# Optimization experiments

Measured on AMD Instinct MI355X. Metric: run time of the kernel, lower is better.

## Reference

```python
import jax, jax.numpy as jnp
import numpy as np

N_CLASS = 85
BLANK = N_CLASS - 1  # blank_index = n_class - 1
ALPHA = 0.05
B, T, D = 4096, 96, 64


def setup_inputs() -> dict:
    key = jax.random.key(0)
    k1, k2, k3, k4 = jax.random.split(key, 4)
    preds = jax.random.normal(k1, (B, T, N_CLASS), dtype=jnp.float32)
    features = jax.random.normal(k2, (B, T, D), dtype=jnp.float32)
    labels = jax.random.randint(k3, (B, T), 0, N_CLASS, dtype=jnp.int32)
    centers = jax.random.normal(k4, (N_CLASS, D), dtype=jnp.float32) * 0.01
    return {"preds": preds, "features": features, "labels": labels, "centers": centers}


def _char_mask(pred_labels):
    # CTC collapse: keep non-blank positions that are the last of a repeat run.
    is_char = pred_labels != BLANK
    rep = pred_labels[:, :-1] == pred_labels[:, 1:]          # [B, T-1]
    tail = pred_labels[:, :1] > BLANK                         # always False (as in source)
    char_rep = jnp.concatenate([rep, tail], axis=1)           # [B, T]
    return is_char & jnp.logical_not(char_rep)


def reference(preds, features, labels, centers):
    # preds:    [B, T, n_class] softmax/logits -> argmax decode
    # features: [B, T, feat_dims]
    # labels:   [B, T] int, char label aligned to each timestep
    pred_labels = jnp.argmax(preds, axis=-1)                  # [B, T]
    mask = _char_mask(pred_labels).astype(features.dtype)     # [B, T] ragged-as-mask

    centers_batch = centers[labels]                           # gather -> [B, T, D]
    diff = centers_batch - features                           # [B, T, D]

    # tf.nn.l2_loss = sum(x^2)/2, restricted to valid char positions
    loss = 0.5 * jnp.sum(mask * jnp.sum(diff * diff, axis=-1))

    # unique_with_counts analog: per-class counts of valid char positions
    labels_flat = labels.reshape(-1)
    mask_flat = mask.reshape(-1)
    counts = jax.ops.segment_sum(mask_flat, labels_flat, num_segments=N_CLASS)  # [n_class]
    appear = counts[labels]                                   # [B, T]

    # alpha * diff / (1 + appear_times), zeroed outside char positions
    delta = ALPHA * diff * (mask / (1.0 + appear))[..., None]  # [B, T, D]

    # scatter_nd: centers.assign_sub(scatter of per-char deltas)
    upd = jax.ops.segment_sum(delta.reshape(-1, D), labels_flat, num_segments=N_CLASS)
    new_centers = centers - upd                               # [n_class, D]
    return loss, new_centers
```

## Files before the change

### kernel.cpp

```cpp
#include <hip/hip_runtime.h>
#include <cstdint>

#define BB     4096
#define TT     96
#define NC     85
#define BLANKC 84
#define DD     64
#define ALPHA  0.05f
#define BT     (BB * TT)
#define SLICE_F (NC * 17)
#define NF4    (TT * NC / 4)

template<int C0, int C1>
__device__ inline void scanR(const float* __restrict__ row, float& bv, int& bc) {
    bv = row[C0]; bc = C0;
#pragma unroll
    for (int c = C0 + 1; c < C1; ++c) {
        float v = row[c];
        if (v > bv) { bv = v; bc = c; }
    }
}

__global__ __launch_bounds__(512) void k_amask(const float4* __restrict__ p4,
                                               const int* __restrict__ labels,
                                               unsigned* __restrict__ labm,
                                               int* __restrict__ hpartT,
                                               float* __restrict__ out) {
    __shared__ float rows[TT * NC];
    __shared__ float sv[4 * TT];
    __shared__ int   sc[4 * TT];
    __shared__ int   pls[TT];
    __shared__ int   h[NC];
    int tid = threadIdx.x;
    int b   = blockIdx.x;
    if (tid < NC) h[tid] = 0;
    if (b == 0 && tid == 480) out[0] = 0.f;

    const float4* src = p4 + (size_t)b * NF4;
    float4* r4 = (float4*)rows;
    float4 v[4];
#pragma unroll
    for (int k = 0; k < 4; ++k)
        v[k] = src[min(tid + k * 512, NF4 - 1)];
#pragma unroll
    for (int k = 0; k < 4; ++k) {
        int i = tid + k * 512;
        if (i < NF4) r4[i] = v[k];
    }
    __syncthreads();

    int q = tid >> 7, r = tid & 127;
    if (r < TT) {
        const float* row = rows + r * NC;
        float bv; int bc;
        switch (q) {
            case 0:  scanR< 0, 22>(row, bv, bc); break;
            case 1:  scanR<22, 43>(row, bv, bc); break;
            case 2:  scanR<43, 64>(row, bv, bc); break;
            default: scanR<64, 85>(row, bv, bc); break;
        }
        sv[q * TT + r] = bv; sc[q * TT + r] = bc;
    }
    __syncthreads();
    if (tid < TT) {
        float bv = sv[tid]; int bc = sc[tid];
#pragma unroll
        for (int qq = 1; qq < 4; ++qq) {
            float v2 = sv[qq * TT + tid];
            int   c2 = sc[qq * TT + tid];
            if (v2 > bv) { bv = v2; bc = c2; }
        }
        pls[tid] = bc;
    }
    __syncthreads();
    if (tid < TT) {
        int p = pls[tid];
        int m = (p != BLANKC) && (tid == TT - 1 || p != pls[tid + 1]);
        int lab = labels[b * TT + tid];
        labm[b * TT + tid] = (unsigned)lab | ((unsigned)m << 31);
        atomicAdd(&h[lab], m);
    }
    __syncthreads();
    if (tid < NC) hpartT[tid * BB + b] = h[tid];
}

__global__ __launch_bounds__(512, 6) void k_main(const float* __restrict__ feat,
                                                 const unsigned* __restrict__ labm,
                                                 float* __restrict__ updp,
                                                 float* __restrict__ lossp, int nb) {
    __shared__ float sl[8 * SLICE_F];
    __shared__ float lred[8];
    int tid = threadIdx.x;
    for (int i = tid; i < 8 * SLICE_F; i += 512) sl[i] = 0.f;
    __syncthreads();

    int lane = tid & 63;
    int w    = tid >> 6;
    int dq   = w & 3;
    int wg   = w >> 2;
    int sub  = lane >> 4;
    int l16  = lane & 15;
    float* slice = sl + w * SLICE_F;

    int ppc = BT / (nb * 2);
    int p0  = (blockIdx.x * 2 + wg) * ppc;
    int nss = ppc / 16;
    const float* fbase = feat + dq * 16 + l16;

    float lsum = 0.f;
    float fA0, fA1, fA2, fA3, fB0, fB1, fB2, fB3;
    uint4 lA0, lA1, lA2, lA3, lB0, lB1, lB2, lB3;

#define ISSUE(P, f0, f1, f2, f3, q0, q1, q2, q3) do {            \
    int _p = (P);                                                \
    q0 = *(const uint4*)(labm + _p);                             \
    q1 = *(const uint4*)(labm + _p + 4);                         \
    q2 = *(const uint4*)(labm + _p + 8);                         \
    q3 = *(const uint4*)(labm + _p + 12);                        \
    f0 = fbase[(size_t)(_p + sub) * DD];                         \
    f1 = fbase[(size_t)(_p + 4 + sub) * DD];                     \
    f2 = fbase[(size_t)(_p + 8 + sub) * DD];                     \
    f3 = fbase[(size_t)(_p + 12 + sub) * DD];                    \
} while (0)

#define SUBSTEP(lv, fc) do {                                     \
    unsigned a0 = lv.x & 0x7fffffffu, a1 = lv.y & 0x7fffffffu,   \
             a2 = lv.z & 0x7fffffffu, a3 = lv.w & 0x7fffffffu;   \
    bool dup = (a0 == a1) | (a0 == a2) | (a0 == a3) |            \
               (a1 == a2) | (a1 == a3) | (a2 == a3);             \
    unsigned lw = (sub & 2) ? ((sub & 1) ? lv.w : lv.z)          \
                            : ((sub & 1) ? lv.y : lv.x);         \
    float m = (float)(lw >> 31);                                 \
    int  la = (int)(lw & 0x7fffffffu);                           \
    float c = m * (fc);                                          \
    lsum = fmaf(c, (fc), lsum);                                  \
    int a = la * 17 + l16;                                       \
    if (!dup) slice[a] += c;                                     \
    else      atomicAdd(&slice[a], c);                           \
} while (0)

    ISSUE(p0, fA0, fA1, fA2, fA3, lA0, lA1, lA2, lA3);
    for (int ss = 0; ss < nss; ss += 2) {
        if (ss + 1 < nss)
            ISSUE(p0 + (ss + 1) * 16, fB0, fB1, fB2, fB3, lB0, lB1, lB2, lB3);
        SUBSTEP(lA0, fA0); SUBSTEP(lA1, fA1);
        SUBSTEP(lA2, fA2); SUBSTEP(lA3, fA3);
        if (ss + 1 < nss) {
            if (ss + 2 < nss)
                ISSUE(p0 + (ss + 2) * 16, fA0, fA1, fA2, fA3, lA0, lA1, lA2, lA3);
            SUBSTEP(lB0, fB0); SUBSTEP(lB1, fB1);
            SUBSTEP(lB2, fB2); SUBSTEP(lB3, fB3);
        }
    }
#undef ISSUE
#undef SUBSTEP
    __syncthreads();

    float* myp = updp + (size_t)blockIdx.x * (NC * DD);
    for (int i = tid; i < NC * DD; i += 512) {
        int r = i >> 6, d = i & 63;
        int qq = d >> 4, d16 = d & 15;
        myp[i] = sl[qq * SLICE_F + r * 17 + d16] +
                 sl[(qq + 4) * SLICE_F + r * 17 + d16];
    }
#pragma unroll
    for (int off = 32; off; off >>= 1) lsum += __shfl_xor(lsum, off);
    if (lane == 0) lred[w] = lsum;
    __syncthreads();
    if (tid == 0) {
        float s = 0.f;
#pragma unroll
        for (int ww = 0; ww < 8; ++ww) s += lred[ww];
        lossp[blockIdx.x] = s;
    }
}

__global__ __launch_bounds__(256) void k_reduce(const float* __restrict__ updp,
                                                const float* __restrict__ lossp,
                                                const float* __restrict__ centers,
                                                const int* __restrict__ hpartT,
                                                float* __restrict__ out, int nb) {
    __shared__ float sred[256];
    __shared__ float sr[4];
    __shared__ int   scnt;
    int tid = threadIdx.x;
    int bid = blockIdx.x;
    if (bid < NC * 4) {
        int j = bid >> 2, q = bid & 3;
        int cs = 0;
        for (int t = tid; t < BB; t += 256) cs += hpartT[j * BB + t];
#pragma unroll
        for (int off = 32; off; off >>= 1) cs += __shfl_xor(cs, off);
        int lane = tid & 63, wv = tid >> 6;
        if (lane == 0) ((int*)sred)[wv] = cs;
        __syncthreads();
        if (tid == 0)
            scnt = ((int*)sred)[0] + ((int*)sred)[1] +
                   ((int*)sred)[2] + ((int*)sred)[3];
        __syncthreads();
        float cnt = (float)scnt;
        int i = tid & 15;
        int c16 = tid >> 4;
        int per = nb >> 4;
        int col = j * DD + q * 16 + i;
        float s = 0.f;
        for (int b = c16 * per; b < (c16 + 1) * per; ++b)
            s += updp[(size_t)b * (NC * DD) + col];
        sred[tid] = s;
        __syncthreads();
        if (tid < 16) {
            float F = 0.f;
#pragma unroll
            for (int cc = 0; cc < 16; ++cc) F += sred[cc * 16 + i];
            float c   = centers[col];
            float scale = ALPHA / (1.f + cnt);
            out[1 + col] = c - scale * (cnt * c - F);
            float lp = cnt * c * c - 2.f * c * F;
#pragma unroll
            for (int off = 8; off; off >>= 1) lp += __shfl_xor(lp, off);
            if (i == 0) atomicAdd(&out[0], 0.5f * lp);
        }
    } else {
        float s = 0.f;
        for (int t = tid; t < nb; t += 256) s += lossp[t];
#pragma unroll
        for (int off = 32; off; off >>= 1) s += __shfl_xor(s, off);
        int lane = tid & 63, wv = tid >> 6;
        if (lane == 0) sr[wv] = s;
        __syncthreads();
        if (tid == 0) atomicAdd(&out[0], 0.5f * (sr[0] + sr[1] + sr[2] + sr[3]));
    }
}

extern "C" void kernel_launch(void* const* d_in, const int* in_sizes, int n_in,
                              void* d_out, int out_size, void* d_ws, size_t ws_size,
                              hipStream_t stream) {
    const float* preds    = (const float*)d_in[0];
    const float* features = (const float*)d_in[1];
    const int*   labels   = (const int*)d_in[2];
    const float* centers  = (const float*)d_in[3];
    float* out = (float*)d_out;

    char* ws = (char*)d_ws;
    unsigned* labm = (unsigned*)ws;
    int* hpartT    = (int*)(ws + 4 * (size_t)BT);
    size_t off0 = 4 * (size_t)BT + (size_t)NC * BB * 4 + 512;

    int nb = 768;
    while (nb > 16 && off0 + (size_t)nb * 4 + 512 +
                      (size_t)nb * NC * DD * 4 > ws_size)
        nb >>= 1;
    float* lossp = (float*)(ws + off0);
    float* updp  = (float*)(ws + off0 + (size_t)nb * 4 + 512);

    k_amask<<<BB, 512, 0, stream>>>((const float4*)preds, labels, labm,
                                    hpartT, out);
    k_main<<<nb, 512, 0, stream>>>(features, labm, updp, lossp, nb);
    k_reduce<<<NC * 4 + 1, 256, 0, stream>>>(updp, lossp, centers, hpartT,
                                             out, nb);
}
```

Baseline: 83.29 us.

## Fuse argmax-mask and feature accumulation into one kernel per four sequences

Merges the argmax/CTC-mask kernel and the feature-accumulation kernel into a single kernel in which each block handles four sequences. Each wave computes the argmax with shuffle reductions, and the label/mask words and duplicate flags live in shared memory instead of a global buffer. This removes one kernel launch and the global round-trip of the label-mask array, and overlaps the first feature loads with the preds scan. The trade-offs are 1024 partial-update blocks for the reduce kernel to sum (it summed 768 before), no ws_size fallback, and higher per-block shared memory and register use.

```diff
diff --git a/kernel.cpp b/kernel.cpp
--- a/kernel.cpp
+++ b/kernel.cpp
@@ -9,91 +9,53 @@
 #define ALPHA  0.05f
 #define BT     (BB * TT)
 #define SLICE_F (NC * 17)
-#define NF4    (TT * NC / 4)
-
-template<int C0, int C1>
-__device__ inline void scanR(const float* __restrict__ row, float& bv, int& bc) {
-    bv = row[C0]; bc = C0;
-#pragma unroll
-    for (int c = C0 + 1; c < C1; ++c) {
-        float v = row[c];
-        if (v > bv) { bv = v; bc = c; }
-    }
-}
-
-__global__ __launch_bounds__(512) void k_amask(const float4* __restrict__ p4,
-                                               const int* __restrict__ labels,
-                                               unsigned* __restrict__ labm,
-                                               int* __restrict__ hpartT,
-                                               float* __restrict__ out) {
-    __shared__ float rows[TT * NC];
-    __shared__ float sv[4 * TT];
-    __shared__ int   sc[4 * TT];
-    __shared__ int   pls[TT];
+#define GPB    4
+#define PPB    (GPB * TT)
+#define NBLKF  (BB / GPB)
+#define NSS    12
+
+__device__ inline void pload(const float* __restrict__ pb, int r0, int lane,
+                             float* arr) {
+#pragma unroll
+    for (int rr = 0; rr < 4; ++rr) {
+        const float* rp = pb + (size_t)(r0 + rr) * NC;
+        arr[rr * 2]     = rp[lane];
+        arr[rr * 2 + 1] = (lane < NC - 64) ? rp[64 + lane] : -3.4e38f;
+    }
+}
+
+__device__ inline void preduce(int* __restrict__ pls, int r0, int lane,
+                               const float* arr) {
+#pragma unroll
+    for (int rr = 0; rr < 4; ++rr) {
+        float v; int bi;
+        if (arr[rr * 2 + 1] > arr[rr * 2]) { v = arr[rr * 2 + 1]; bi = lane + 64; }
+        else                               { v = arr[rr * 2];     bi = lane; }
+#pragma unroll
+        for (int off = 32; off; off >>= 1) {
+            float ov = __shfl_xor(v, off);
+            int   oi = __shfl_xor(bi, off);
+            if (ov > v || (ov == v && oi < bi)) { v = ov; bi = oi; }
+        }
+        if (lane == 0) pls[r0 + rr] = bi;
+    }
+}
+
+__global__ __launch_bounds__(512, 6) void k_fused(const float* __restrict__ preds,
+                                                  const int* __restrict__ labels,
+                                                  const float* __restrict__ feat,
+                                                  float* __restrict__ updp,
+                                                  int* __restrict__ hpartT,
+                                                  float* __restrict__ lossp,
+                                                  float* __restrict__ out) {
+    __shared__ float sl[8 * SLICE_F];
+    __shared__ __align__(16) unsigned labm_w[PPB];
+    __shared__ int   pls[PPB];
     __shared__ int   h[NC];
-    int tid = threadIdx.x;
-    int b   = blockIdx.x;
-    if (tid < NC) h[tid] = 0;
-    if (b == 0 && tid == 480) out[0] = 0.f;
-
-    const float4* src = p4 + (size_t)b * NF4;
-    float4* r4 = (float4*)rows;
-    float4 v[4];
-#pragma unroll
-    for (int k = 0; k < 4; ++k)
-        v[k] = src[min(tid + k * 512, NF4 - 1)];
-#pragma unroll
-    for (int k = 0; k < 4; ++k) {
-        int i = tid + k * 512;
-        if (i < NF4) r4[i] = v[k];
-    }
-    __syncthreads();
-
-    int q = tid >> 7, r = tid & 127;
-    if (r < TT) {
-        const float* row = rows + r * NC;
-        float bv; int bc;
-        switch (q) {
-            case 0:  scanR< 0, 22>(row, bv, bc); break;
-            case 1:  scanR<22, 43>(row, bv, bc); break;
-            case 2:  scanR<43, 64>(row, bv, bc); break;
-            default: scanR<64, 85>(row, bv, bc); break;
-        }
-        sv[q * TT + r] = bv; sc[q * TT + r] = bc;
-    }
-    __syncthreads();
-    if (tid < TT) {
-        float bv = sv[tid]; int bc = sc[tid];
-#pragma unroll
-        for (int qq = 1; qq < 4; ++qq) {
-            float v2 = sv[qq * TT + tid];
-            int   c2 = sc[qq * TT + tid];
-            if (v2 > bv) { bv = v2; bc = c2; }
-        }
-        pls[tid] = bc;
-    }
-    __syncthreads();
-    if (tid < TT) {
-        int p = pls[tid];
-        int m = (p != BLANKC) && (tid == TT - 1 || p != pls[tid + 1]);
-        int lab = labels[b * TT + tid];
-        labm[b * TT + tid] = (unsigned)lab | ((unsigned)m << 31);
-        atomicAdd(&h[lab], m);
-    }
-    __syncthreads();
-    if (tid < NC) hpartT[tid * BB + b] = h[tid];
-}
-
-__global__ __launch_bounds__(512, 6) void k_main(const float* __restrict__ feat,
-                                                 const unsigned* __restrict__ labm,
-                                                 float* __restrict__ updp,
-                                                 float* __restrict__ lossp, int nb) {
-    __shared__ float sl[8 * SLICE_F];
     __shared__ float lred[8];
-    int tid = threadIdx.x;
-    for (int i = tid; i < 8 * SLICE_F; i += 512) sl[i] = 0.f;
-    __syncthreads();
-
+
+    int tid  = threadIdx.x;
+    int blk  = blockIdx.x;
     int lane = tid & 63;
     int w    = tid >> 6;
     int dq   = w & 3;
@@ -102,36 +64,74 @@
     int l16  = lane & 15;
     float* slice = sl + w * SLICE_F;
 
-    int ppc = BT / (nb * 2);
-    int p0  = (blockIdx.x * 2 + wg) * ppc;
-    int nss = ppc / 16;
-    const float* fbase = feat + dq * 16 + l16;
-
-    float lsum = 0.f;
+    for (int i = tid; i < 8 * SLICE_F; i += 512) sl[i] = 0.f;
+    if (tid < NC) h[tid] = 0;
+    if (blk == 0 && tid == 500) out[0] = 0.f;
+    int labreg = (tid < PPB) ? labels[blk * PPB + tid] : 0;
+
+    const float* fbase = feat + (size_t)blk * PPB * DD + dq * 16 + l16;
+    int p0 = wg * (NSS * 16);
+    int g0 = wg * (NSS * 4);
     float fA0, fA1, fA2, fA3, fB0, fB1, fB2, fB3;
-    uint4 lA0, lA1, lA2, lA3, lB0, lB1, lB2, lB3;
-
-#define ISSUE(P, f0, f1, f2, f3, q0, q1, q2, q3) do {            \
+    float fC0, fC1, fC2, fC3, fD0, fD1, fD2, fD3;
+
+#define ISSUE_F(P, f0, f1, f2, f3) do {                          \
     int _p = (P);                                                \
-    q0 = *(const uint4*)(labm + _p);                             \
-    q1 = *(const uint4*)(labm + _p + 4);                         \
-    q2 = *(const uint4*)(labm + _p + 8);                         \
-    q3 = *(const uint4*)(labm + _p + 12);                        \
     f0 = fbase[(size_t)(_p + sub) * DD];                         \
     f1 = fbase[(size_t)(_p + 4 + sub) * DD];                     \
     f2 = fbase[(size_t)(_p + 8 + sub) * DD];                     \
     f3 = fbase[(size_t)(_p + 12 + sub) * DD];                    \
 } while (0)
 
-#define SUBSTEP(lv, fc) do {                                     \
-    unsigned a0 = lv.x & 0x7fffffffu, a1 = lv.y & 0x7fffffffu,   \
-             a2 = lv.z & 0x7fffffffu, a3 = lv.w & 0x7fffffffu;   \
-    bool dup = (a0 == a1) | (a0 == a2) | (a0 == a3) |            \
-               (a1 == a2) | (a1 == a3) | (a2 == a3);             \
+    ISSUE_F(p0,      fA0, fA1, fA2, fA3);
+    ISSUE_F(p0 + 16, fB0, fB1, fB2, fB3);
+    ISSUE_F(p0 + 32, fC0, fC1, fC2, fC3);
+    ISSUE_F(p0 + 48, fD0, fD1, fD2, fD3);
+
+    {
+        const float* pb = preds + (size_t)blk * PPB * NC;
+        int rb = w * 48;
+        float av[8], bv[8];
+        pload(pb, rb, lane, av);
+        for (int g = 0; g < 12; g += 2) {
+            pload(pb, rb + (g + 1) * 4, lane, bv);
+            preduce(pls, rb + g * 4, lane, av);
+            if (g + 2 < 12) pload(pb, rb + (g + 2) * 4, lane, av);
+            preduce(pls, rb + (g + 1) * 4, lane, bv);
+        }
+    }
+    __syncthreads();
+
+    if (tid < PPB) {
+        int p  = pls[tid];
+        int lp = tid % TT;
+        int m  = (p != BLANKC) && (lp == TT - 1 || p != pls[tid + 1]);
+        labm_w[tid] = (unsigned)labreg | ((unsigned)m << 31);
+        atomicAdd(&h[labreg], m);
+    }
+    __syncthreads();
+
+    if (tid < PPB / 4) {
+        unsigned a0 = labm_w[tid * 4]     & 0x7fffffffu;
+        unsigned a1 = labm_w[tid * 4 + 1] & 0x7fffffffu;
+        unsigned a2 = labm_w[tid * 4 + 2] & 0x7fffffffu;
+        unsigned a3 = labm_w[tid * 4 + 3] & 0x7fffffffu;
+        bool dup = (a0 == a1) | (a0 == a2) | (a0 == a3) |
+                   (a1 == a2) | (a1 == a3) | (a2 == a3);
+        if (dup) labm_w[tid * 4] |= 0x40000000u;
+    }
+    __syncthreads();
+
+    const uint4* labm4 = (const uint4*)labm_w;
+    float lsum = 0.f;
+
+#define SUBSTEP(GI, fc) do {                                     \
+    uint4 lv = labm4[GI];                                        \
+    bool dup = (lv.x >> 30) & 1u;                                \
     unsigned lw = (sub & 2) ? ((sub & 1) ? lv.w : lv.z)          \
                             : ((sub & 1) ? lv.y : lv.x);         \
     float m = (float)(lw >> 31);                                 \
-    int  la = (int)(lw & 0x7fffffffu);                           \
+    int  la = (int)(lw & 0x3fffffffu);                           \
     float c = m * (fc);                                          \
     lsum = fmaf(c, (fc), lsum);                                  \
     int a = la * 17 + l16;                                       \
@@ -139,30 +139,33 @@
     else      atomicAdd(&slice[a], c);                           \
 } while (0)
 
-    ISSUE(p0, fA0, fA1, fA2, fA3, lA0, lA1, lA2, lA3);
-    for (int ss = 0; ss < nss; ss += 2) {
-        if (ss + 1 < nss)
-            ISSUE(p0 + (ss + 1) * 16, fB0, fB1, fB2, fB3, lB0, lB1, lB2, lB3);
-        SUBSTEP(lA0, fA0); SUBSTEP(lA1, fA1);
-        SUBSTEP(lA2, fA2); SUBSTEP(lA3, fA3);
-        if (ss + 1 < nss) {
-            if (ss + 2 < nss)
-                ISSUE(p0 + (ss + 2) * 16, fA0, fA1, fA2, fA3, lA0, lA1, lA2, lA3);
-            SUBSTEP(lB0, fB0); SUBSTEP(lB1, fB1);
-            SUBSTEP(lB2, fB2); SUBSTEP(lB3, fB3);
-        }
-    }
-#undef ISSUE
+#pragma unroll
+    for (int ss = 0; ss < NSS; ss += 4) {
+        SUBSTEP(g0 + ss * 4 + 0, fA0); SUBSTEP(g0 + ss * 4 + 1, fA1);
+        SUBSTEP(g0 + ss * 4 + 2, fA2); SUBSTEP(g0 + ss * 4 + 3, fA3);
+        if (ss + 4 < NSS) ISSUE_F(p0 + (ss + 4) * 16, fA0, fA1, fA2, fA3);
+        SUBSTEP(g0 + (ss + 1) * 4 + 0, fB0); SUBSTEP(g0 + (ss + 1) * 4 + 1, fB1);
+        SUBSTEP(g0 + (ss + 1) * 4 + 2, fB2); SUBSTEP(g0 + (ss + 1) * 4 + 3, fB3);
+        if (ss + 5 < NSS) ISSUE_F(p0 + (ss + 5) * 16, fB0, fB1, fB2, fB3);
+        SUBSTEP(g0 + (ss + 2) * 4 + 0, fC0); SUBSTEP(g0 + (ss + 2) * 4 + 1, fC1);
+        SUBSTEP(g0 + (ss + 2) * 4 + 2, fC2); SUBSTEP(g0 + (ss + 2) * 4 + 3, fC3);
+        if (ss + 6 < NSS) ISSUE_F(p0 + (ss + 6) * 16, fC0, fC1, fC2, fC3);
+        SUBSTEP(g0 + (ss + 3) * 4 + 0, fD0); SUBSTEP(g0 + (ss + 3) * 4 + 1, fD1);
+        SUBSTEP(g0 + (ss + 3) * 4 + 2, fD2); SUBSTEP(g0 + (ss + 3) * 4 + 3, fD3);
+        if (ss + 7 < NSS) ISSUE_F(p0 + (ss + 7) * 16, fD0, fD1, fD2, fD3);
+    }
+#undef ISSUE_F
 #undef SUBSTEP
     __syncthreads();
 
-    float* myp = updp + (size_t)blockIdx.x * (NC * DD);
+    float* myp = updp + (size_t)blk * (NC * DD);
     for (int i = tid; i < NC * DD; i += 512) {
         int r = i >> 6, d = i & 63;
         int qq = d >> 4, d16 = d & 15;
         myp[i] = sl[qq * SLICE_F + r * 17 + d16] +
                  sl[(qq + 4) * SLICE_F + r * 17 + d16];
     }
+    if (tid < NC) hpartT[tid * NBLKF + blk] = h[tid];
 #pragma unroll
     for (int off = 32; off; off >>= 1) lsum += __shfl_xor(lsum, off);
     if (lane == 0) lred[w] = lsum;
@@ -171,7 +174,7 @@
         float s = 0.f;
 #pragma unroll
         for (int ww = 0; ww < 8; ++ww) s += lred[ww];
-        lossp[blockIdx.x] = s;
+        lossp[blk] = s;
     }
 }
 
@@ -179,7 +182,7 @@
                                                 const float* __restrict__ lossp,
                                                 const float* __restrict__ centers,
                                                 const int* __restrict__ hpartT,
-                                                float* __restrict__ out, int nb) {
+                                                float* __restrict__ out) {
     __shared__ float sred[256];
     __shared__ float sr[4];
     __shared__ int   scnt;
@@ -188,7 +191,7 @@
     if (bid < NC * 4) {
         int j = bid >> 2, q = bid & 3;
         int cs = 0;
-        for (int t = tid; t < BB; t += 256) cs += hpartT[j * BB + t];
+        for (int t = tid; t < NBLKF; t += 256) cs += hpartT[j * NBLKF + t];
 #pragma unroll
         for (int off = 32; off; off >>= 1) cs += __shfl_xor(cs, off);
         int lane = tid & 63, wv = tid >> 6;
@@ -201,7 +204,7 @@
         float cnt = (float)scnt;
         int i = tid & 15;
         int c16 = tid >> 4;
-        int per = nb >> 4;
+        int per = NBLKF >> 4;
         int col = j * DD + q * 16 + i;
         float s = 0.f;
         for (int b = c16 * per; b < (c16 + 1) * per; ++b)
@@ -222,7 +225,7 @@
         }
     } else {
         float s = 0.f;
-        for (int t = tid; t < nb; t += 256) s += lossp[t];
+        for (int t = tid; t < NBLKF; t += 256) s += lossp[t];
 #pragma unroll
         for (int off = 32; off; off >>= 1) s += __shfl_xor(s, off);
         int lane = tid & 63, wv = tid >> 6;
@@ -242,20 +245,12 @@
     float* out = (float*)d_out;
 
     char* ws = (char*)d_ws;
-    unsigned* labm = (unsigned*)ws;
-    int* hpartT    = (int*)(ws + 4 * (size_t)BT);
-    size_t off0 = 4 * (size_t)BT + (size_t)NC * BB * 4 + 512;
-
-    int nb = 768;
-    while (nb > 16 && off0 + (size_t)nb * 4 + 512 +
-                      (size_t)nb * NC * DD * 4 > ws_size)
-        nb >>= 1;
-    float* lossp = (float*)(ws + off0);
-    float* updp  = (float*)(ws + off0 + (size_t)nb * 4 + 512);
-
-    k_amask<<<BB, 512, 0, stream>>>((const float4*)preds, labels, labm,
-                                    hpartT, out);
-    k_main<<<nb, 512, 0, stream>>>(features, labm, updp, lossp, nb);
-    k_reduce<<<NC * 4 + 1, 256, 0, stream>>>(updp, lossp, centers, hpartT,
-                                             out, nb);
-}
+    float* updp   = (float*)ws;
+    int*   hpartT = (int*)(ws + (size_t)NBLKF * NC * DD * 4);
+    float* lossp  = (float*)(ws + (size_t)NBLKF * NC * DD * 4
+                                + (size_t)NC * NBLKF * 4);
+
+    k_fused<<<NBLKF, 512, 0, stream>>>(preds, labels, features,
+                                       updp, hpartT, lossp, out);
+    k_reduce<<<NC * 4 + 1, 256, 0, stream>>>(updp, lossp, centers, hpartT, out);
+}
```

Result: slower. 207.7 us (+149.4%).

## Give each wave its own rows for argmax and reduce with shuffles

Applied to the files above, without the earlier changes.

Each of the 8 wavefronts now loads its own 12 rows of preds into shared memory and computes the argmax for those rows. Four lanes per row each scan a quarter of the classes and combine through xor shuffles. This removes two block-wide barriers and the shared-memory partial-result arrays, and the labels load is issued early so it overlaps with the preds load. The new column loop is not unrolled, which may cost some instruction-level parallelism. Only 48 of 64 lanes per wave do useful work in the scan.

```diff
diff --git a/kernel.cpp b/kernel.cpp
--- a/kernel.cpp
+++ b/kernel.cpp
@@ -11,74 +11,63 @@
 #define SLICE_F (NC * 17)
 #define NF4    (TT * NC / 4)
 
-template<int C0, int C1>
-__device__ inline void scanR(const float* __restrict__ row, float& bv, int& bc) {
-    bv = row[C0]; bc = C0;
-#pragma unroll
-    for (int c = C0 + 1; c < C1; ++c) {
-        float v = row[c];
-        if (v > bv) { bv = v; bc = c; }
-    }
-}
-
 __global__ __launch_bounds__(512) void k_amask(const float4* __restrict__ p4,
                                                const int* __restrict__ labels,
                                                unsigned* __restrict__ labm,
                                                int* __restrict__ hpartT,
                                                float* __restrict__ out) {
     __shared__ float rows[TT * NC];
-    __shared__ float sv[4 * TT];
-    __shared__ int   sc[4 * TT];
     __shared__ int   pls[TT];
     __shared__ int   h[NC];
-    int tid = threadIdx.x;
-    int b   = blockIdx.x;
+    int tid  = threadIdx.x;
+    int b    = blockIdx.x;
+    int lane = tid & 63;
+    int w    = tid >> 6;
     if (tid < NC) h[tid] = 0;
     if (b == 0 && tid == 480) out[0] = 0.f;
-
-    const float4* src = p4 + (size_t)b * NF4;
-    float4* r4 = (float4*)rows;
-    float4 v[4];
-#pragma unroll
-    for (int k = 0; k < 4; ++k)
-        v[k] = src[min(tid + k * 512, NF4 - 1)];
-#pragma unroll
-    for (int k = 0; k < 4; ++k) {
-        int i = tid + k * 512;
-        if (i < NF4) r4[i] = v[k];
-    }
-    __syncthreads();
-
-    int q = tid >> 7, r = tid & 127;
-    if (r < TT) {
-        const float* row = rows + r * NC;
-        float bv; int bc;
-        switch (q) {
-            case 0:  scanR< 0, 22>(row, bv, bc); break;
-            case 1:  scanR<22, 43>(row, bv, bc); break;
-            case 2:  scanR<43, 64>(row, bv, bc); break;
-            default: scanR<64, 85>(row, bv, bc); break;
-        }
-        sv[q * TT + r] = bv; sc[q * TT + r] = bc;
-    }
-    __syncthreads();
-    if (tid < TT) {
-        float bv = sv[tid]; int bc = sc[tid];
-#pragma unroll
-        for (int qq = 1; qq < 4; ++qq) {
-            float v2 = sv[qq * TT + tid];
-            int   c2 = sc[qq * TT + tid];
-            if (v2 > bv) { bv = v2; bc = c2; }
-        }
-        pls[tid] = bc;
+    int labreg = (tid < TT) ? labels[b * TT + tid] : 0;
+
+    {
+        const float4* src = p4 + (size_t)b * NF4 + 255 * w;
+        float4* dst = (float4*)(rows + (size_t)w * 12 * NC);
+        float4 v0 = src[lane];
+        float4 v1 = src[lane + 64];
+        float4 v2 = src[lane + 128];
+        float4 v3 = (lane < 63) ? src[lane + 192] : v2;
+        dst[lane]       = v0;
+        dst[lane + 64]  = v1;
+        dst[lane + 128] = v2;
+        if (lane < 63) dst[lane + 192] = v3;
+    }
+    {
+        const int c0t[4] = {0, 22, 43, 64};
+        const int c1t[4] = {22, 43, 64, 85};
+        int r  = lane >> 2;
+        int q  = lane & 3;
+        float bv = -3.4e38f; int bc = 127;
+        if (lane < 48) {
+            const float* row = rows + (w * 12 + r) * NC;
+            int c0 = c0t[q], c1 = c1t[q];
+            bv = row[c0]; bc = c0;
+            for (int c = c0 + 1; c < c1; ++c) {
+                float v = row[c];
+                if (v > bv) { bv = v; bc = c; }
+            }
+        }
+#pragma unroll
+        for (int m = 1; m <= 2; m <<= 1) {
+            float ov = __shfl_xor(bv, m);
+            int   oc = __shfl_xor(bc, m);
+            if (ov > bv || (ov == bv && oc < bc)) { bv = ov; bc = oc; }
+        }
+        if (lane < 48 && (lane & 3) == 0) pls[w * 12 + r] = bc;
     }
     __syncthreads();
     if (tid < TT) {
         int p = pls[tid];
         int m = (p != BLANKC) && (tid == TT - 1 || p != pls[tid + 1]);
-        int lab = labels[b * TT + tid];
-        labm[b * TT + tid] = (unsigned)lab | ((unsigned)m << 31);
-        atomicAdd(&h[lab], m);
+        labm[b * TT + tid] = (unsigned)labreg | ((unsigned)m << 31);
+        atomicAdd(&h[labreg], m);
     }
     __syncthreads();
     if (tid < NC) hpartT[tid * BB + b] = h[tid];
```

After: 85.42 us. +2.6%, slower.
